# Kernel optimization log

Measured on AMD Instinct MI355X. Metric: run time of the kernel, lower is better.

## Reference

```python
import jax, jax.numpy as jnp
import numpy as np
from jax import lax

N_EMBD = 4096
N_EXPERTS = 64


def setup_inputs() -> dict:
    key = jax.random.key(0)
    kx, kw = jax.random.split(key)
    x = jax.random.normal(kx, (4, 4096, N_EMBD), dtype=jnp.float32)
    # nn.Linear(n_embd, n_experts, bias=False) -> weight shape [n_experts, n_embd]
    W = jax.random.normal(kw, (N_EXPERTS, N_EMBD), dtype=jnp.float32) * (1.0 / np.sqrt(N_EMBD))
    return {"x": x, "W": W}


def reference(x, W):
    # logits = x @ W^T : [B, S, n_experts]
    logits = jnp.einsum('bsd,ed->bse', x, W)
    topk_vals, topk_idx = lax.top_k(logits, 2)  # [B, S, 2]
    gates = jax.nn.softmax(topk_vals, axis=-1)  # softmax over just the top-2 values
    return (topk_idx, gates)
```

## Files before the change

### kernel.cpp

```cpp
#include <hip/hip_runtime.h>
#include <math.h>

#define N_EMBD    4096
#define N_EXPERTS 64
#define N_TOKENS  16384
#define TAU       1e-3f
#define BM        16
#define BK        128
#define NTILES    (N_EMBD / BK)

typedef __attribute__((ext_vector_type(8))) short bf16x8;
typedef __attribute__((ext_vector_type(4))) float f32x4;

#define MFMA16 __builtin_amdgcn_mfma_f32_16x16x32_bf16

struct hl_pair { unsigned h, l; };

__device__ __forceinline__ hl_pair split_pair(float f0, float f1) {
    unsigned u0 = __builtin_bit_cast(unsigned, f0);
    unsigned u1 = __builtin_bit_cast(unsigned, f1);
    unsigned r0 = u0 + 0x7FFFu + ((u0 >> 16) & 1u);
    unsigned r1 = u1 + 0x7FFFu + ((u1 >> 16) & 1u);
    hl_pair p;
    p.h = (r0 >> 16) | (r1 & 0xFFFF0000u);
    float h0 = __builtin_bit_cast(float, r0 & 0xFFFF0000u);
    float h1 = __builtin_bit_cast(float, r1 & 0xFFFF0000u);
    float l0 = f0 - h0;
    float l1 = f1 - h1;
    unsigned v0 = __builtin_bit_cast(unsigned, l0);
    unsigned v1 = __builtin_bit_cast(unsigned, l1);
    unsigned s0 = v0 + 0x7FFFu + ((v0 >> 16) & 1u);
    unsigned s1 = v1 + 0x7FFFu + ((v1 >> 16) & 1u);
    p.l = (s0 >> 16) | (s1 & 0xFFFF0000u);
    return p;
}

__global__ void w_pack_bf16(const float* __restrict__ W,
                            uint4* __restrict__ Bpack,
                            int* __restrict__ flags) {
    int tid = blockIdx.x * blockDim.x + threadIdx.x;
    if (tid == 0) flags[0] = 0;
    int lane = tid & 63;
    int nt   = (tid >> 6) & 3;
    int ks   = tid >> 8;
    int e = nt * 16 + (lane & 15);
    int k = ks * 32 + ((lane >> 4) << 3);
    const float* src = W + (size_t)e * N_EMBD + k;
    uint4 hp, lp;
    hl_pair p0 = split_pair(src[0], src[1]);
    hl_pair p1 = split_pair(src[2], src[3]);
    hl_pair p2 = split_pair(src[4], src[5]);
    hl_pair p3 = split_pair(src[6], src[7]);
    hp.x = p0.h; lp.x = p0.l;
    hp.y = p1.h; lp.y = p1.l;
    hp.z = p2.h; lp.z = p2.l;
    hp.w = p3.h; lp.w = p3.l;
    size_t F = (size_t)ks * 8 + nt * 2;
    Bpack[F * 64 + lane]       = hp;
    Bpack[(F + 1) * 64 + lane] = lp;
}

__device__ __forceinline__ void store_split(char* buf, int off, f32x4 v) {
    hl_pair p01 = split_pair(v.x, v.y);
    hl_pair p23 = split_pair(v.z, v.w);
    uint2 hw, lw;
    hw.x = p01.h; hw.y = p23.h;
    lw.x = p01.l; lw.y = p23.l;
    *(uint2*)(buf + off)        = hw;
    *(uint2*)(buf + off + 4096) = lw;
}

__global__ __launch_bounds__(256, 4) void router_fused(
        const float* __restrict__ x,
        const uint4* __restrict__ Bpack,
        float* __restrict__ out,
        int* __restrict__ flags) {
    __shared__ __align__(16) char ldsA[2 * 8192];
    __shared__ float red[BM][64];

    const int tid  = threadIdx.x;
    const int lane = tid & 63;
    const int w    = tid >> 6;
    const int tok0 = blockIdx.x * BM;

    const int k4   = tid & 31;
    const int row0 = tid >> 5;
    const f32x4* g0 = (const f32x4*)x + (size_t)(tok0 + row0) * (N_EMBD / 4) + k4;
    const f32x4* g1 = g0 + 8 * (N_EMBD / 4);
    const int swz = (row0 & 7) << 4;
    const int wo0 = ((row0    ) * 256 + k4 * 8) ^ swz;
    const int wo1 = ((row0 + 8) * 256 + k4 * 8) ^ swz;

    const int l15 = lane & 15, l16 = lane >> 4;
    const int ro_base = l15 * 256 + l16 * 16;
    const int swz_r   = (l15 & 7) << 4;
    const int off0 = (ro_base +   0) ^ swz_r;
    const int off1 = (ro_base +  64) ^ swz_r;
    const int off2 = (ro_base + 128) ^ swz_r;
    const int off3 = (ro_base + 192) ^ swz_r;

    f32x4 acc = {0.f, 0.f, 0.f, 0.f};

    f32x4 r0 = g0[0];
    f32x4 r1 = g1[0];
    store_split(ldsA, wo0, r0);
    store_split(ldsA, wo1, r1);
    r0 = g0[BK / 4];
    r1 = g1[BK / 4];
    asm volatile("s_waitcnt lgkmcnt(0)" ::: "memory");
    __builtin_amdgcn_s_barrier();
    __builtin_amdgcn_sched_barrier(0);

    for (int t = 0; t < NTILES; ++t) {
        char* bufr = ldsA + (t & 1) * 8192;
        char* bufw = ldsA + ((t & 1) ^ 1) * 8192;

        const uint4* bq = Bpack + ((size_t)(t * 4) * 8 + w * 2) * 64 + lane;
        uint4 bh0 = bq[0];    uint4 bl0 = bq[64];
        uint4 bh1 = bq[512];  uint4 bl1 = bq[576];
        uint4 bh2 = bq[1024]; uint4 bl2 = bq[1088];
        uint4 bh3 = bq[1536]; uint4 bl3 = bq[1600];

        bf16x8 ah, al;
        ah = *(const bf16x8*)(bufr + off0);
        al = *(const bf16x8*)(bufr + off0 + 4096);
        acc = MFMA16(ah, __builtin_bit_cast(bf16x8, bh0), acc, 0, 0, 0);
        acc = MFMA16(ah, __builtin_bit_cast(bf16x8, bl0), acc, 0, 0, 0);
        acc = MFMA16(al, __builtin_bit_cast(bf16x8, bh0), acc, 0, 0, 0);
        ah = *(const bf16x8*)(bufr + off1);
        al = *(const bf16x8*)(bufr + off1 + 4096);
        acc = MFMA16(ah, __builtin_bit_cast(bf16x8, bh1), acc, 0, 0, 0);
        acc = MFMA16(ah, __builtin_bit_cast(bf16x8, bl1), acc, 0, 0, 0);
        acc = MFMA16(al, __builtin_bit_cast(bf16x8, bh1), acc, 0, 0, 0);
        ah = *(const bf16x8*)(bufr + off2);
        al = *(const bf16x8*)(bufr + off2 + 4096);
        acc = MFMA16(ah, __builtin_bit_cast(bf16x8, bh2), acc, 0, 0, 0);
        acc = MFMA16(ah, __builtin_bit_cast(bf16x8, bl2), acc, 0, 0, 0);
        acc = MFMA16(al, __builtin_bit_cast(bf16x8, bh2), acc, 0, 0, 0);
        ah = *(const bf16x8*)(bufr + off3);
        al = *(const bf16x8*)(bufr + off3 + 4096);
        acc = MFMA16(ah, __builtin_bit_cast(bf16x8, bh3), acc, 0, 0, 0);
        acc = MFMA16(ah, __builtin_bit_cast(bf16x8, bl3), acc, 0, 0, 0);
        acc = MFMA16(al, __builtin_bit_cast(bf16x8, bh3), acc, 0, 0, 0);

        if (t + 1 < NTILES) {
            store_split(bufw, wo0, r0);
            store_split(bufw, wo1, r1);
            if (t + 2 < NTILES) {
                r0 = g0[(t + 2) * (BK / 4)];
                r1 = g1[(t + 2) * (BK / 4)];
            }
            asm volatile("s_waitcnt lgkmcnt(0)" ::: "memory");
            __builtin_amdgcn_s_barrier();
            __builtin_amdgcn_sched_barrier(0);
        }
    }

    const int rb = l16 << 2;
#pragma unroll
    for (int j = 0; j < 4; ++j)
        red[rb + j][w * 16 + l15] = acc[j];
    __syncthreads();

    for (int tt = 0; tt < 4; ++tt) {
        const int t = w * 4 + tt;
        float v = red[t][lane];

        float m1 = v; int i1 = lane;
#pragma unroll
        for (int off = 32; off; off >>= 1) {
            float ov = __shfl_xor(m1, off); int oi = __shfl_xor(i1, off);
            if (ov > m1 || (ov == m1 && oi < i1)) { m1 = ov; i1 = oi; }
        }
        float m2 = (lane == i1) ? -INFINITY : v; int i2 = lane;
#pragma unroll
        for (int off = 32; off; off >>= 1) {
            float ov = __shfl_xor(m2, off); int oi = __shfl_xor(i2, off);
            if (ov > m2 || (ov == m2 && oi < i2)) { m2 = ov; i2 = oi; }
        }
        float m3 = (lane == i1 || lane == i2) ? -INFINITY : v;
#pragma unroll
        for (int off = 32; off; off >>= 1)
            m3 = fmaxf(m3, __shfl_xor(m3, off));

        if (lane == 0) {
            const int tok = tok0 + t;
            float e2  = __expf(m2 - m1);
            float inv = 1.0f / (1.0f + e2);
            float2 idx = make_float2((float)i1, (float)i2);
            float2 gts = make_float2(inv, e2 * inv);
            *(float2*)(out + 2 * tok) = idx;
            *(float2*)(out + 2 * N_TOKENS + 2 * tok) = gts;
            if ((m1 - m2 < TAU) || (m2 - m3 < TAU)) {
                int p = atomicAdd(flags, 1);
                if (p < N_TOKENS) flags[1 + p] = tok;
            }
        }
    }
}

__global__ __launch_bounds__(256) void refine(const float* __restrict__ x,
                                              const float* __restrict__ W,
                                              const int* __restrict__ flags,
                                              float* __restrict__ out) {
    __shared__ double redd[64];
    const int lane = threadIdx.x & 63;
    const int wv   = threadIdx.x >> 6;
    int cnt = flags[0];
    if (cnt > N_TOKENS) cnt = N_TOKENS;

    for (int i = blockIdx.x; i < cnt; i += gridDim.x) {
        const int tok = flags[1 + i];
        const float4* xr4 = (const float4*)(x + (size_t)tok * N_EMBD);
#pragma unroll
        for (int ee = 0; ee < 16; ++ee) {
            const int e = wv * 16 + ee;
            const float4* wr = (const float4*)(W + (size_t)e * N_EMBD);
            double acc = 0.0;
#pragma unroll 4
            for (int c = 0; c < 16; ++c) {
                float4 xv = xr4[c * 64 + lane];
                float4 wq = wr[c * 64 + lane];
                acc += (double)xv.x * wq.x + (double)xv.y * wq.y
                     + (double)xv.z * wq.z + (double)xv.w * wq.w;
            }
#pragma unroll
            for (int off = 32; off; off >>= 1)
                acc += __shfl_xor(acc, off);
            if (lane == 0) redd[e] = acc;
        }
        __syncthreads();
        if (wv == 0) {
            double v = redd[lane];
            double m1 = v; int i1 = lane;
#pragma unroll
            for (int off = 32; off; off >>= 1) {
                double ov = __shfl_xor(m1, off); int oi = __shfl_xor(i1, off);
                if (ov > m1 || (ov == m1 && oi < i1)) { m1 = ov; i1 = oi; }
            }
            double m2 = (lane == i1) ? -INFINITY : v; int i2 = lane;
#pragma unroll
            for (int off = 32; off; off >>= 1) {
                double ov = __shfl_xor(m2, off); int oi = __shfl_xor(i2, off);
                if (ov > m2 || (ov == m2 && oi < i2)) { m2 = ov; i2 = oi; }
            }
            if (lane == 0) {
                double e2  = exp(m2 - m1);
                double inv = 1.0 / (1.0 + e2);
                out[2 * tok + 0] = (float)i1;
                out[2 * tok + 1] = (float)i2;
                out[2 * N_TOKENS + 2 * tok + 0] = (float)inv;
                out[2 * N_TOKENS + 2 * tok + 1] = (float)(e2 * inv);
            }
        }
        __syncthreads();
    }
}

extern "C" void kernel_launch(void* const* d_in, const int* in_sizes, int n_in,
                              void* d_out, int out_size, void* d_ws, size_t ws_size,
                              hipStream_t stream) {
    const float* x = (const float*)d_in[0];
    const float* W = (const float*)d_in[1];
    float* out = (float*)d_out;

    uint4* Bpack = (uint4*)d_ws;
    int*   flags = (int*)((char*)d_ws + (2u << 20));

    w_pack_bf16 <<<128, 256, 0, stream>>>(W, Bpack, flags);
    router_fused<<<N_TOKENS / BM, 256, 0, stream>>>(x, Bpack, out, flags);
    refine      <<<128, 256, 0, stream>>>(x, W, flags, out);
}
```

Measured before the change: 105.7 us.

## Stream raw fp32 x tiles into LDS asynchronously with triple buffering

Replaces the register-staged load, split-to-bf16 and LDS store of activation tiles with direct global-to-LDS async copies of raw fp32 data into a three-deep ring buffer. The hi/lo bf16 split now happens after reading from LDS, just before the MFMAs. The aim is to drop the register round trip and overlap global loads with compute more deeply. In exchange, LDS use and LDS read traffic double per tile, since fp32 is stored instead of packed bf16. The vmcnt wait accounting also has to stay correct with the B-operand global loads issued in the same loop.

```diff
diff --git a/kernel.cpp b/kernel.cpp
--- a/kernel.cpp
+++ b/kernel.cpp
@@ -8,9 +8,11 @@
 #define BM        16
 #define BK        128
 #define NTILES    (N_EMBD / BK)
+#define TILE_B    8192
 
 typedef __attribute__((ext_vector_type(8))) short bf16x8;
 typedef __attribute__((ext_vector_type(4))) float f32x4;
+typedef __attribute__((ext_vector_type(4))) unsigned u32x4;
 
 #define MFMA16 __builtin_amdgcn_mfma_f32_16x16x32_bf16
 
@@ -33,6 +35,25 @@
     unsigned s1 = v1 + 0x7FFFu + ((v1 >> 16) & 1u);
     p.l = (s0 >> 16) | (s1 & 0xFFFF0000u);
     return p;
+}
+
+__device__ __forceinline__ void split_tile(f32x4 A0, f32x4 A1,
+                                           bf16x8& ah, bf16x8& al) {
+    u32x4 hu, lu;
+    hl_pair p;
+    p = split_pair(A0.x, A0.y); hu.x = p.h; lu.x = p.l;
+    p = split_pair(A0.z, A0.w); hu.y = p.h; lu.y = p.l;
+    p = split_pair(A1.x, A1.y); hu.z = p.h; lu.z = p.l;
+    p = split_pair(A1.z, A1.w); hu.w = p.h; lu.w = p.l;
+    ah = __builtin_bit_cast(bf16x8, hu);
+    al = __builtin_bit_cast(bf16x8, lu);
+}
+
+__device__ __forceinline__ void async_copy16(void* lds_dst, const void* gsrc) {
+    __builtin_amdgcn_global_load_lds(
+        (const __attribute__((address_space(1))) unsigned int*)gsrc,
+        (__attribute__((address_space(3))) unsigned int*)lds_dst,
+        16, 0, 0);
 }
 
 __global__ void w_pack_bf16(const float* __restrict__ W,
@@ -60,60 +81,50 @@
     Bpack[(F + 1) * 64 + lane] = lp;
 }
 
-__device__ __forceinline__ void store_split(char* buf, int off, f32x4 v) {
-    hl_pair p01 = split_pair(v.x, v.y);
-    hl_pair p23 = split_pair(v.z, v.w);
-    uint2 hw, lw;
-    hw.x = p01.h; hw.y = p23.h;
-    lw.x = p01.l; lw.y = p23.l;
-    *(uint2*)(buf + off)        = hw;
-    *(uint2*)(buf + off + 4096) = lw;
-}
-
 __global__ __launch_bounds__(256, 4) void router_fused(
         const float* __restrict__ x,
         const uint4* __restrict__ Bpack,
         float* __restrict__ out,
         int* __restrict__ flags) {
-    __shared__ __align__(16) char ldsA[2 * 8192];
+    __shared__ __align__(16) char ldsA[3 * TILE_B];
     __shared__ float red[BM][64];
 
     const int tid  = threadIdx.x;
     const int lane = tid & 63;
     const int w    = tid >> 6;
     const int tok0 = blockIdx.x * BM;
-
-    const int k4   = tid & 31;
-    const int row0 = tid >> 5;
-    const f32x4* g0 = (const f32x4*)x + (size_t)(tok0 + row0) * (N_EMBD / 4) + k4;
-    const f32x4* g1 = g0 + 8 * (N_EMBD / 4);
-    const int swz = (row0 & 7) << 4;
-    const int wo0 = ((row0    ) * 256 + k4 * 8) ^ swz;
-    const int wo1 = ((row0 + 8) * 256 + k4 * 8) ^ swz;
-
     const int l15 = lane & 15, l16 = lane >> 4;
-    const int ro_base = l15 * 256 + l16 * 16;
-    const int swz_r   = (l15 & 7) << 4;
-    const int off0 = (ro_base +   0) ^ swz_r;
-    const int off1 = (ro_base +  64) ^ swz_r;
-    const int off2 = (ro_base + 128) ^ swz_r;
-    const int off3 = (ro_base + 192) ^ swz_r;
+
+    const int P0   = w * 2048 + lane * 16;
+    const int P1   = P0 + 1024;
+    const int row0 = P0 >> 9;
+    const int row1 = P1 >> 9;
+    const int c0   = (P0 & 511) ^ ((row0 & 7) << 4);
+    const int c1   = (P1 & 511) ^ ((row1 & 7) << 4);
+    const float* gA0 = x + (size_t)(tok0 + row0) * N_EMBD + (c0 >> 2);
+    const float* gA1 = x + (size_t)(tok0 + row1) * N_EMBD + (c1 >> 2);
+
+    const int swz_r = (l15 & 7) << 4;
+    int roff[8];
+#pragma unroll
+    for (int ksl = 0; ksl < 4; ++ksl) {
+        roff[2 * ksl]     = l15 * 512 + ((l16 * 32 + ksl * 128)      ^ swz_r);
+        roff[2 * ksl + 1] = l15 * 512 + ((l16 * 32 + ksl * 128 + 16) ^ swz_r);
+    }
 
     f32x4 acc = {0.f, 0.f, 0.f, 0.f};
 
-    f32x4 r0 = g0[0];
-    f32x4 r1 = g1[0];
-    store_split(ldsA, wo0, r0);
-    store_split(ldsA, wo1, r1);
-    r0 = g0[BK / 4];
-    r1 = g1[BK / 4];
-    asm volatile("s_waitcnt lgkmcnt(0)" ::: "memory");
+    async_copy16(ldsA + 0 * TILE_B + w * 2048,        gA0);
+    async_copy16(ldsA + 0 * TILE_B + w * 2048 + 1024, gA1);
+    async_copy16(ldsA + 1 * TILE_B + w * 2048,        gA0 + 128);
+    async_copy16(ldsA + 1 * TILE_B + w * 2048 + 1024, gA1 + 128);
+    asm volatile("s_waitcnt vmcnt(2)" ::: "memory");
     __builtin_amdgcn_s_barrier();
     __builtin_amdgcn_sched_barrier(0);
 
     for (int t = 0; t < NTILES; ++t) {
-        char* bufr = ldsA + (t & 1) * 8192;
-        char* bufw = ldsA + ((t & 1) ^ 1) * 8192;
+        char* bufR = ldsA + (t % 3) * TILE_B;
+        char* bufW = ldsA + ((t + 2) % 3) * TILE_B;
 
         const uint4* bq = Bpack + ((size_t)(t * 4) * 8 + w * 2) * 64 + lane;
         uint4 bh0 = bq[0];    uint4 bl0 = bq[64];
@@ -121,36 +132,44 @@
         uint4 bh2 = bq[1024]; uint4 bl2 = bq[1088];
         uint4 bh3 = bq[1536]; uint4 bl3 = bq[1600];
 
+        if (t + 2 < NTILES) {
+            async_copy16(bufW + w * 2048,        gA0 + (t + 2) * 128);
+            async_copy16(bufW + w * 2048 + 1024, gA1 + (t + 2) * 128);
+        }
+
         bf16x8 ah, al;
-        ah = *(const bf16x8*)(bufr + off0);
-        al = *(const bf16x8*)(bufr + off0 + 4096);
+        f32x4 a0, a1;
+        a0 = *(const f32x4*)(bufR + roff[0]);
+        a1 = *(const f32x4*)(bufR + roff[1]);
+        split_tile(a0, a1, ah, al);
         acc = MFMA16(ah, __builtin_bit_cast(bf16x8, bh0), acc, 0, 0, 0);
         acc = MFMA16(ah, __builtin_bit_cast(bf16x8, bl0), acc, 0, 0, 0);
         acc = MFMA16(al, __builtin_bit_cast(bf16x8, bh0), acc, 0, 0, 0);
-        ah = *(const bf16x8*)(bufr + off1);
-        al = *(const bf16x8*)(bufr + off1 + 4096);
+        a0 = *(const f32x4*)(bufR + roff[2]);
+        a1 = *(const f32x4*)(bufR + roff[3]);
+        split_tile(a0, a1, ah, al);
         acc = MFMA16(ah, __builtin_bit_cast(bf16x8, bh1), acc, 0, 0, 0);
         acc = MFMA16(ah, __builtin_bit_cast(bf16x8, bl1), acc, 0, 0, 0);
         acc = MFMA16(al, __builtin_bit_cast(bf16x8, bh1), acc, 0, 0, 0);
-        ah = *(const bf16x8*)(bufr + off2);
-        al = *(const bf16x8*)(bufr + off2 + 4096);
+        a0 = *(const f32x4*)(bufR + roff[4]);
+        a1 = *(const f32x4*)(bufR + roff[5]);
+        split_tile(a0, a1, ah, al);
         acc = MFMA16(ah, __builtin_bit_cast(bf16x8, bh2), acc, 0, 0, 0);
         acc = MFMA16(ah, __builtin_bit_cast(bf16x8, bl2), acc, 0, 0, 0);
         acc = MFMA16(al, __builtin_bit_cast(bf16x8, bh2), acc, 0, 0, 0);
-        ah = *(const bf16x8*)(bufr + off3);
-        al = *(const bf16x8*)(bufr + off3 + 4096);
+        a0 = *(const f32x4*)(bufR + roff[6]);
+        a1 = *(const f32x4*)(bufR + roff[7]);
+        split_tile(a0, a1, ah, al);
         acc = MFMA16(ah, __builtin_bit_cast(bf16x8, bh3), acc, 0, 0, 0);
         acc = MFMA16(ah, __builtin_bit_cast(bf16x8, bl3), acc, 0, 0, 0);
         acc = MFMA16(al, __builtin_bit_cast(bf16x8, bh3), acc, 0, 0, 0);
 
-        if (t + 1 < NTILES) {
-            store_split(bufw, wo0, r0);
-            store_split(bufw, wo1, r1);
-            if (t + 2 < NTILES) {
-                r0 = g0[(t + 2) * (BK / 4)];
-                r1 = g1[(t + 2) * (BK / 4)];
-            }
-            asm volatile("s_waitcnt lgkmcnt(0)" ::: "memory");
+        if (t < NTILES - 2) {
+            asm volatile("s_waitcnt vmcnt(2)" ::: "memory");
+            __builtin_amdgcn_s_barrier();
+            __builtin_amdgcn_sched_barrier(0);
+        } else if (t == NTILES - 2) {
+            asm volatile("s_waitcnt vmcnt(0)" ::: "memory");
             __builtin_amdgcn_s_barrier();
             __builtin_amdgcn_sched_barrier(0);
         }
```

After: 136.3 us. 1.29x slower.

## Prefetch W tiles one step ahead with ping-pong registers and MFMA priority

Applied to the files above, without the earlier changes.

Unrolls the K loop by two and double-buffers the packed weight fragments in registers, so the B loads for tile t+1 are issued before computing tile t instead of right before use. Sched barriers pin the issue order, and s_setprio raises wave priority around the MFMA blocks. The cost being attacked is exposed global/L2 latency on the weight loads in each iteration. In exchange it holds 16 more uint4 registers live, which may pressure the occupancy target of 4 blocks per CU.

```diff
diff --git a/kernel.cpp b/kernel.cpp
--- a/kernel.cpp
+++ b/kernel.cpp
@@ -82,6 +82,7 @@
     const int lane = tid & 63;
     const int w    = tid >> 6;
     const int tok0 = blockIdx.x * BM;
+    const int l15 = lane & 15, l16 = lane >> 4;
 
     const int k4   = tid & 31;
     const int row0 = tid >> 5;
@@ -91,70 +92,96 @@
     const int wo0 = ((row0    ) * 256 + k4 * 8) ^ swz;
     const int wo1 = ((row0 + 8) * 256 + k4 * 8) ^ swz;
 
-    const int l15 = lane & 15, l16 = lane >> 4;
+    const int swz_r = (l15 & 7) << 4;
     const int ro_base = l15 * 256 + l16 * 16;
-    const int swz_r   = (l15 & 7) << 4;
     const int off0 = (ro_base +   0) ^ swz_r;
     const int off1 = (ro_base +  64) ^ swz_r;
     const int off2 = (ro_base + 128) ^ swz_r;
     const int off3 = (ro_base + 192) ^ swz_r;
 
     f32x4 acc = {0.f, 0.f, 0.f, 0.f};
-
-    f32x4 r0 = g0[0];
-    f32x4 r1 = g1[0];
-    store_split(ldsA, wo0, r0);
-    store_split(ldsA, wo1, r1);
-    r0 = g0[BK / 4];
-    r1 = g1[BK / 4];
+    f32x4 r0, r1;
+    uint4 bA0h, bA0l, bA1h, bA1l, bA2h, bA2l, bA3h, bA3l;
+    uint4 bB0h, bB0l, bB1h, bB1l, bB2h, bB2l, bB3h, bB3l;
+
+    char* buf0 = ldsA;
+    char* buf1 = ldsA + 8192;
+
+#define LOADA(t) { r0 = g0[(t) * 32]; r1 = g1[(t) * 32]; }
+#define STOREA(buf) { store_split(buf, wo0, r0); store_split(buf, wo1, r1); }
+#define LOADB(P, tt) { const uint4* bq = Bpack                                \
+        + ((size_t)((tt) * 4) * 8 + w * 2) * 64 + lane;                       \
+    P##0h = bq[0];    P##0l = bq[64];                                         \
+    P##1h = bq[512];  P##1l = bq[576];                                        \
+    P##2h = bq[1024]; P##2l = bq[1088];                                       \
+    P##3h = bq[1536]; P##3l = bq[1600]; }
+#define COMPUTE(bufR, P) {                                                    \
+    bf16x8 ah, al, bh, bl;                                                    \
+    __builtin_amdgcn_s_setprio(1);                                            \
+    bh = __builtin_bit_cast(bf16x8, P##0h); bl = __builtin_bit_cast(bf16x8, P##0l); \
+    ah = *(const bf16x8*)((bufR) + off0);                                     \
+    al = *(const bf16x8*)((bufR) + off0 + 4096);                              \
+    acc = MFMA16(ah, bh, acc, 0, 0, 0);                                       \
+    acc = MFMA16(ah, bl, acc, 0, 0, 0);                                       \
+    acc = MFMA16(al, bh, acc, 0, 0, 0);                                       \
+    bh = __builtin_bit_cast(bf16x8, P##1h); bl = __builtin_bit_cast(bf16x8, P##1l); \
+    ah = *(const bf16x8*)((bufR) + off1);                                     \
+    al = *(const bf16x8*)((bufR) + off1 + 4096);                              \
+    acc = MFMA16(ah, bh, acc, 0, 0, 0);                                       \
+    acc = MFMA16(ah, bl, acc, 0, 0, 0);                                       \
+    acc = MFMA16(al, bh, acc, 0, 0, 0);                                       \
+    bh = __builtin_bit_cast(bf16x8, P##2h); bl = __builtin_bit_cast(bf16x8, P##2l); \
+    ah = *(const bf16x8*)((bufR) + off2);                                     \
+    al = *(const bf16x8*)((bufR) + off2 + 4096);                              \
+    acc = MFMA16(ah, bh, acc, 0, 0, 0);                                       \
+    acc = MFMA16(ah, bl, acc, 0, 0, 0);                                       \
+    acc = MFMA16(al, bh, acc, 0, 0, 0);                                       \
+    bh = __builtin_bit_cast(bf16x8, P##3h); bl = __builtin_bit_cast(bf16x8, P##3l); \
+    ah = *(const bf16x8*)((bufR) + off3);                                     \
+    al = *(const bf16x8*)((bufR) + off3 + 4096);                              \
+    acc = MFMA16(ah, bh, acc, 0, 0, 0);                                       \
+    acc = MFMA16(ah, bl, acc, 0, 0, 0);                                       \
+    acc = MFMA16(al, bh, acc, 0, 0, 0);                                       \
+    __builtin_amdgcn_s_setprio(0); }
+
+    LOADA(0);
+    STOREA(buf0);
+    LOADB(bA, 0);
+    LOADA(1);
+    __builtin_amdgcn_sched_barrier(0);
     asm volatile("s_waitcnt lgkmcnt(0)" ::: "memory");
     __builtin_amdgcn_s_barrier();
     __builtin_amdgcn_sched_barrier(0);
 
-    for (int t = 0; t < NTILES; ++t) {
-        char* bufr = ldsA + (t & 1) * 8192;
-        char* bufw = ldsA + ((t & 1) ^ 1) * 8192;
-
-        const uint4* bq = Bpack + ((size_t)(t * 4) * 8 + w * 2) * 64 + lane;
-        uint4 bh0 = bq[0];    uint4 bl0 = bq[64];
-        uint4 bh1 = bq[512];  uint4 bl1 = bq[576];
-        uint4 bh2 = bq[1024]; uint4 bl2 = bq[1088];
-        uint4 bh3 = bq[1536]; uint4 bl3 = bq[1600];
-
-        bf16x8 ah, al;
-        ah = *(const bf16x8*)(bufr + off0);
-        al = *(const bf16x8*)(bufr + off0 + 4096);
-        acc = MFMA16(ah, __builtin_bit_cast(bf16x8, bh0), acc, 0, 0, 0);
-        acc = MFMA16(ah, __builtin_bit_cast(bf16x8, bl0), acc, 0, 0, 0);
-        acc = MFMA16(al, __builtin_bit_cast(bf16x8, bh0), acc, 0, 0, 0);
-        ah = *(const bf16x8*)(bufr + off1);
-        al = *(const bf16x8*)(bufr + off1 + 4096);
-        acc = MFMA16(ah, __builtin_bit_cast(bf16x8, bh1), acc, 0, 0, 0);
-        acc = MFMA16(ah, __builtin_bit_cast(bf16x8, bl1), acc, 0, 0, 0);
-        acc = MFMA16(al, __builtin_bit_cast(bf16x8, bh1), acc, 0, 0, 0);
-        ah = *(const bf16x8*)(bufr + off2);
-        al = *(const bf16x8*)(bufr + off2 + 4096);
-        acc = MFMA16(ah, __builtin_bit_cast(bf16x8, bh2), acc, 0, 0, 0);
-        acc = MFMA16(ah, __builtin_bit_cast(bf16x8, bl2), acc, 0, 0, 0);
-        acc = MFMA16(al, __builtin_bit_cast(bf16x8, bh2), acc, 0, 0, 0);
-        ah = *(const bf16x8*)(bufr + off3);
-        al = *(const bf16x8*)(bufr + off3 + 4096);
-        acc = MFMA16(ah, __builtin_bit_cast(bf16x8, bh3), acc, 0, 0, 0);
-        acc = MFMA16(ah, __builtin_bit_cast(bf16x8, bl3), acc, 0, 0, 0);
-        acc = MFMA16(al, __builtin_bit_cast(bf16x8, bh3), acc, 0, 0, 0);
-
-        if (t + 1 < NTILES) {
-            store_split(bufw, wo0, r0);
-            store_split(bufw, wo1, r1);
-            if (t + 2 < NTILES) {
-                r0 = g0[(t + 2) * (BK / 4)];
-                r1 = g1[(t + 2) * (BK / 4)];
-            }
+    for (int t = 0; t < NTILES; t += 2) {
+        LOADB(bB, t + 1);
+        __builtin_amdgcn_sched_barrier(0);
+        COMPUTE(buf0, bA);
+        STOREA(buf1);
+        if (t + 2 < NTILES) LOADA(t + 2);
+        __builtin_amdgcn_sched_barrier(0);
+        asm volatile("s_waitcnt lgkmcnt(0)" ::: "memory");
+        __builtin_amdgcn_s_barrier();
+        __builtin_amdgcn_sched_barrier(0);
+
+        if (t + 2 < NTILES) {
+            LOADB(bA, t + 2);
+            __builtin_amdgcn_sched_barrier(0);
+            COMPUTE(buf1, bB);
+            STOREA(buf0);
+            if (t + 3 < NTILES) LOADA(t + 3);
+            __builtin_amdgcn_sched_barrier(0);
             asm volatile("s_waitcnt lgkmcnt(0)" ::: "memory");
             __builtin_amdgcn_s_barrier();
             __builtin_amdgcn_sched_barrier(0);
+        } else {
+            COMPUTE(buf1, bB);
         }
     }
+#undef LOADA
+#undef STOREA
+#undef LOADB
+#undef COMPUTE
 
     const int rb = l16 << 2;
 #pragma unroll
```

After: 109.9 us. 1.04x slower.
